# Performance work log

Hardware: AMD Instinct MI355X
Metric: run time of the kernel (lower is better)

Reference implementation:

```python
import jax, jax.numpy as jnp
import numpy as np

B, N = 16384, 128

def setup_inputs() -> dict:
    key = jax.random.key(0)
    k1, k2, k3, k4, k5, k6, k7, k8, k9 = jax.random.split(key, 9)
    float_feats = jax.random.normal(k1, (B, N, 5), dtype=jnp.float32)
    # valid TM atomic numbers: 21..30 and 39..48 -> sample uniformly from [21,49) then shift the 31..38 band
    z = jax.random.randint(k2, (B, N), 21, 49)
    z = jnp.where((z >= 31) & (z <= 38), z + 10, z)  # keep only valid TM Z values
    etype = jax.random.randint(k3, (B, N), 0, 6)
    elements_info = jnp.concatenate(
        [float_feats, z[..., None].astype(jnp.float32), etype[..., None].astype(jnp.float32)], axis=-1)
    elements_mask = jax.random.randint(k4, (B, N), 0, 2).astype(jnp.int32)
    W = jax.random.normal(k5, (16, 5), dtype=jnp.float32) * (1.0 / np.sqrt(5.0))
    b = jax.random.normal(k6, (16,), dtype=jnp.float32) * 0.02
    TM_emb = jax.random.normal(k7, (21, 8), dtype=jnp.float32)
    NotTM_emb1 = jax.random.normal(k8, (75, 8), dtype=jnp.float32)
    NotTM_emb2 = jax.random.normal(k9, (6, 4), dtype=jnp.float32)
    return {"elements_info": elements_info, "elements_mask": elements_mask,
            "W": W, "b": b, "TM_emb": TM_emb, "NotTM_emb1": NotTM_emb1,
            "NotTM_emb2": NotTM_emb2, "is_tm": 1}

def map_tm(z):
    # 0 -> 0 (masked); 21..30 -> 1..10; 39..48 -> 11..20
    return jnp.where(z <= 0, 0, jnp.where(z <= 30, z - 20, z - 28))

def map_not_tm(z):
    # 0 -> 0; 1..20 -> z; 31..38 -> 21..28; 49..94 -> 29..74
    return jnp.where(z <= 0, 0,
           jnp.where(z <= 20, z,
           jnp.where(z <= 38, z - 31 + 21, z - 49 + 29)))

def reference(elements_info, elements_mask, W, b, TM_emb, NotTM_emb1, NotTM_emb2, is_tm):
    maskf = elements_mask.astype(jnp.float32)[..., None]          # [B,N,1]
    masked = elements_info * maskf                                # [B,N,7]
    float_features = masked[..., :5]
    atomic_num = masked[..., 5].astype(jnp.int32)
    element_type = masked[..., 6].astype(jnp.int32)
    float_feat = jax.nn.relu(jnp.einsum('bnf,of->bno', float_features, W) + b)  # [B,N,16]
    if is_tm:  # static python branch, matching torch's is_tm kwarg
        emb_z = TM_emb[map_tm(atomic_num)]                        # [B,N,8]
        out = jnp.concatenate([float_feat, emb_z], axis=-1)       # [B,N,24]
    else:
        emb_z = NotTM_emb1[map_not_tm(atomic_num)]
        emb_t = NotTM_emb2[element_type]
        out = jnp.concatenate([float_feat, emb_z, emb_t], axis=-1)
    return out * maskf
```

## Files before the change

kernel.cpp:

```cpp
#include <hip/hip_runtime.h>


__global__ __launch_bounds__(256) void tm_kernel(
    const float* __restrict__ info, const int* __restrict__ mask,
    const float* __restrict__ W, const float* __restrict__ bias,
    const float* __restrict__ TM_emb, float* __restrict__ out, int n_elems)
{
    unsigned int gtid = blockIdx.x * blockDim.x + threadIdx.x;
    unsigned int elem = gtid / 3u;
    unsigned int r = gtid - elem * 3u;
    if (elem >= (unsigned int)n_elems) return;

    float m = (float)mask[elem];
    const float* ei = info + (size_t)elem * 7;

    float res[8];
    if (r < 2u) {
        float f0 = ei[0] * m, f1 = ei[1] * m, f2 = ei[2] * m,
              f3 = ei[3] * m, f4 = ei[4] * m;
        int ob = (int)r * 8;
        #pragma unroll
        for (int k = 0; k < 8; ++k) {
            const float* w = W + (size_t)(ob + k) * 5;
            float acc = bias[ob + k];
            acc = fmaf(f0, w[0], acc);
            acc = fmaf(f1, w[1], acc);
            acc = fmaf(f2, w[2], acc);
            acc = fmaf(f3, w[3], acc);
            acc = fmaf(f4, w[4], acc);
            res[k] = fmaxf(acc, 0.0f) * m;
        }
    } else {
        int z = (int)(ei[5] * m);
        int idx = (z <= 0) ? 0 : ((z <= 30) ? z - 20 : z - 28);
        const float4* e = (const float4*)(TM_emb + (size_t)idx * 8);
        float4 a0 = e[0], a1 = e[1];
        res[0] = a0.x * m; res[1] = a0.y * m; res[2] = a0.z * m; res[3] = a0.w * m;
        res[4] = a1.x * m; res[5] = a1.y * m; res[6] = a1.z * m; res[7] = a1.w * m;
    }

    float* op = out + (size_t)elem * 24 + r * 8;
    float4 v0 = make_float4(res[0], res[1], res[2], res[3]);
    float4 v1 = make_float4(res[4], res[5], res[6], res[7]);
    *(float4*)(op) = v0;
    *(float4*)(op + 4) = v1;
}

__global__ __launch_bounds__(256) void nottm_kernel(
    const float* __restrict__ info, const int* __restrict__ mask,
    const float* __restrict__ W, const float* __restrict__ bias,
    const float* __restrict__ emb1, const float* __restrict__ emb2,
    float* __restrict__ out, int n_elems)
{
    int elem = blockIdx.x * blockDim.x + threadIdx.x;
    if (elem >= n_elems) return;
    float m = (float)mask[elem];
    const float* ei = info + (size_t)elem * 7;
    float f[5];
    #pragma unroll
    for (int i = 0; i < 5; ++i) f[i] = ei[i] * m;
    float* op = out + (size_t)elem * 28;
    #pragma unroll
    for (int o = 0; o < 16; ++o) {
        float acc = bias[o];
        #pragma unroll
        for (int k = 0; k < 5; ++k) acc = fmaf(f[k], W[o * 5 + k], acc);
        op[o] = fmaxf(acc, 0.0f) * m;
    }
    int z = (int)(ei[5] * m);
    int idx = (z <= 0) ? 0 : ((z <= 20) ? z : ((z <= 38) ? z - 10 : z - 20));
    #pragma unroll
    for (int k = 0; k < 8; ++k) op[16 + k] = emb1[idx * 8 + k] * m;
    int t = (int)(ei[6] * m);
    #pragma unroll
    for (int k = 0; k < 4; ++k) op[24 + k] = emb2[t * 4 + k] * m;
}

extern "C" void kernel_launch(void* const* d_in, const int* in_sizes, int n_in,
                              void* d_out, int out_size, void* d_ws, size_t ws_size,
                              hipStream_t stream) {
    const float* info   = (const float*)d_in[0];
    const int*   mask   = (const int*)d_in[1];
    const float* W      = (const float*)d_in[2];
    const float* bias   = (const float*)d_in[3];
    const float* TM_emb = (const float*)d_in[4];
    const float* emb1   = (const float*)d_in[5];
    const float* emb2   = (const float*)d_in[6];

    int n_elems = in_sizes[1];
    int width = out_size / n_elems;
    float* out = (float*)d_out;

    if (width == 24) {
        long long threads = (long long)n_elems * 3;
        int blocks = (int)((threads + 255) / 256);
        tm_kernel<<<blocks, 256, 0, stream>>>(info, mask, W, bias, TM_emb, out, n_elems);
    } else {
        int blocks = (n_elems + 255) / 256;
        nottm_kernel<<<blocks, 256, 0, stream>>>(info, mask, W, bias, emb1, emb2, out, n_elems);
    }
}
```

Baseline: 307.2 us.

## Compute one element per thread and stage output through LDS for coalesced stores

Each thread now computes all 24 outputs of one element instead of splitting the work across three threads. The results are written to a padded shared-memory buffer and then copied out as fully coalesced float4 stores after a block barrier. This removes redundant per-element loads of mask and info and the divide-by-3 indexing, and packs the global writes contiguously. In exchange it adds shared-memory traffic, a __syncthreads, and higher register use from holding 16 outputs per thread.

```diff
diff --git a/kernel.cpp b/kernel.cpp
--- a/kernel.cpp
+++ b/kernel.cpp
@@ -1,49 +1,60 @@
 #include <hip/hip_runtime.h>
 
+
+__device__ __forceinline__ float4 f4scale(float4 a, float s) {
+    return make_float4(a.x * s, a.y * s, a.z * s, a.w * s);
+}
 
 __global__ __launch_bounds__(256) void tm_kernel(
     const float* __restrict__ info, const int* __restrict__ mask,
     const float* __restrict__ W, const float* __restrict__ bias,
     const float* __restrict__ TM_emb, float* __restrict__ out, int n_elems)
 {
-    unsigned int gtid = blockIdx.x * blockDim.x + threadIdx.x;
-    unsigned int elem = gtid / 3u;
-    unsigned int r = gtid - elem * 3u;
-    if (elem >= (unsigned int)n_elems) return;
+    __shared__ float4 sOut[6 * 257];
 
-    float m = (float)mask[elem];
-    const float* ei = info + (size_t)elem * 7;
+    const int tid = threadIdx.x;
+    const int elem = blockIdx.x * 256 + tid;
 
-    float res[8];
-    if (r < 2u) {
-        float f0 = ei[0] * m, f1 = ei[1] * m, f2 = ei[2] * m,
-              f3 = ei[3] * m, f4 = ei[4] * m;
-        int ob = (int)r * 8;
+    if (elem < n_elems) {
+        const float m = (float)mask[elem];
+        const float* ei = info + (size_t)elem * 7;
+        const float f0 = ei[0] * m, f1 = ei[1] * m, f2 = ei[2] * m,
+                    f3 = ei[3] * m, f4 = ei[4] * m;
+
+        float o[16];
         #pragma unroll
-        for (int k = 0; k < 8; ++k) {
-            const float* w = W + (size_t)(ob + k) * 5;
-            float acc = bias[ob + k];
-            acc = fmaf(f0, w[0], acc);
-            acc = fmaf(f1, w[1], acc);
-            acc = fmaf(f2, w[2], acc);
-            acc = fmaf(f3, w[3], acc);
-            acc = fmaf(f4, w[4], acc);
-            res[k] = fmaxf(acc, 0.0f) * m;
+        for (int k = 0; k < 16; ++k) {
+            float acc = bias[k];
+            acc = fmaf(f0, W[k * 5 + 0], acc);
+            acc = fmaf(f1, W[k * 5 + 1], acc);
+            acc = fmaf(f2, W[k * 5 + 2], acc);
+            acc = fmaf(f3, W[k * 5 + 3], acc);
+            acc = fmaf(f4, W[k * 5 + 4], acc);
+            o[k] = fmaxf(acc, 0.0f) * m;
         }
-    } else {
-        int z = (int)(ei[5] * m);
-        int idx = (z <= 0) ? 0 : ((z <= 30) ? z - 20 : z - 28);
-        const float4* e = (const float4*)(TM_emb + (size_t)idx * 8);
-        float4 a0 = e[0], a1 = e[1];
-        res[0] = a0.x * m; res[1] = a0.y * m; res[2] = a0.z * m; res[3] = a0.w * m;
-        res[4] = a1.x * m; res[5] = a1.y * m; res[6] = a1.z * m; res[7] = a1.w * m;
+        sOut[0 * 257 + tid] = make_float4(o[0],  o[1],  o[2],  o[3]);
+        sOut[1 * 257 + tid] = make_float4(o[4],  o[5],  o[6],  o[7]);
+        sOut[2 * 257 + tid] = make_float4(o[8],  o[9],  o[10], o[11]);
+        sOut[3 * 257 + tid] = make_float4(o[12], o[13], o[14], o[15]);
+
+        const int z = (int)(ei[5] * m);
+        const int idx = (z <= 0) ? 0 : ((z <= 30) ? z - 20 : z - 28);
+        const float4* e4 = (const float4*)(TM_emb + (size_t)idx * 8);
+        sOut[4 * 257 + tid] = f4scale(e4[0], m);
+        sOut[5 * 257 + tid] = f4scale(e4[1], m);
     }
+    __syncthreads();
 
-    float* op = out + (size_t)elem * 24 + r * 8;
-    float4 v0 = make_float4(res[0], res[1], res[2], res[3]);
-    float4 v1 = make_float4(res[4], res[5], res[6], res[7]);
-    *(float4*)(op) = v0;
-    *(float4*)(op + 4) = v1;
+    float4* out4 = (float4*)out + (size_t)blockIdx.x * 1536;
+    const int elem0 = blockIdx.x * 256;
+    #pragma unroll
+    for (int it = 0; it < 6; ++it) {
+        const unsigned int g = it * 256 + tid;
+        const unsigned int e = g / 6u;
+        const unsigned int c = g - e * 6u;
+        if (elem0 + (int)e < n_elems)
+            out4[g] = sOut[c * 257 + e];
+    }
 }
 
 __global__ __launch_bounds__(256) void nottm_kernel(
@@ -92,8 +103,7 @@
     float* out = (float*)d_out;
 
     if (width == 24) {
-        long long threads = (long long)n_elems * 3;
-        int blocks = (int)((threads + 255) / 256);
+        int blocks = (n_elems + 255) / 256;
         tm_kernel<<<blocks, 256, 0, stream>>>(info, mask, W, bias, TM_emb, out, n_elems);
     } else {
         int blocks = (n_elems + 255) / 256;
```

Result: faster. 264.0 us (-14.1%).
